# Optimization experiments

Hardware: AMD Instinct MI355X
Metric: run time of the kernel (lower is better)

Reference implementation:

```python
import jax, jax.numpy as jnp
import numpy as np

B, N, DIM = 2, 2048, 1024
HEADS, DIM_HEAD = 16, 64
ALIBI_HEADS = 8
NUM_MEM_KV = 4
SCALE = DIM_HEAD ** -0.5


def alibi_slopes(n):
    # standard ALiBi geometric slopes for power-of-2 head counts
    start = 2.0 ** (-8.0 / n)
    return jnp.array([start ** (k + 1) for k in range(n)], dtype=jnp.float32)


def alibi_bias(i, j, heads, total_heads):
    # symmetric ALiBi: bias = -|k_pos - q_pos| * slope; unbiased heads padded with zeros at front
    range_q = jnp.arange(j - i, j)          # query absolute positions (offset by mem kv)
    range_k = jnp.arange(j)
    rel = -jnp.abs(range_k[None, :] - range_q[:, None]).astype(jnp.float32)  # [i, j]
    slopes = alibi_slopes(heads)
    bias = slopes[:, None, None] * rel[None]                                  # [heads, i, j]
    pad = jnp.zeros((total_heads - heads, i, j), dtype=bias.dtype)
    return jnp.concatenate([pad, bias], axis=0)                               # [total_heads, i, j]


def setup_inputs() -> dict:
    key = jax.random.key(0)
    ks = jax.random.split(key, 7)
    w = lambda k, s: jax.random.normal(k, s, jnp.float32) * 0.02
    return {
        "x": jax.random.normal(ks[0], (B, N, DIM), jnp.float32),
        "mask": jnp.ones((B, N), dtype=bool),
        "Wq": w(ks[1], (DIM, HEADS * DIM_HEAD)),
        "Wk": w(ks[2], (DIM, HEADS * DIM_HEAD)),
        "Wv": w(ks[3], (DIM, HEADS * DIM_HEAD)),
        "Wo": w(ks[4], (HEADS * DIM_HEAD, DIM)),
        "mem_k": jax.random.normal(ks[5], (HEADS, NUM_MEM_KV, DIM_HEAD), jnp.float32),
        "mem_v": jax.random.normal(ks[6], (HEADS, NUM_MEM_KV, DIM_HEAD), jnp.float32),
    }


def reference(x, mask, Wq, Wk, Wv, Wo, mem_k, mem_v):
    b, n, _ = x.shape
    h, d, m = HEADS, DIM_HEAD, NUM_MEM_KV
    # QKV projections (Linear, no bias)
    q = (x @ Wq).reshape(b, n, h, d).transpose(0, 2, 1, 3)  # [b,h,n,d]
    k = (x @ Wk).reshape(b, n, h, d).transpose(0, 2, 1, 3)
    v = (x @ Wv).reshape(b, n, h, d).transpose(0, 2, 1, 3)
    # prepend learned memory key/values
    k = jnp.concatenate([jnp.broadcast_to(mem_k[None], (b, h, m, d)), k], axis=2)
    v = jnp.concatenate([jnp.broadcast_to(mem_v[None], (b, h, m, d)), v], axis=2)
    i, j = n, n + m
    # input mask padded with True over memory positions
    input_mask = jnp.concatenate([jnp.ones((b, m), dtype=bool), mask], axis=1)  # [b,j]
    # causal mask: key kj attendable by query qi iff kj - (j - i) <= qi (mem keys always visible)
    qpos = jnp.arange(i)[:, None]
    kpos = jnp.arange(j)[None, :]
    causal_allow = (kpos - (j - i)) <= qpos                                      # [i,j]
    allow = input_mask[:, None, None, :] & causal_allow[None, None]              # [b,1,i,j]
    bias = alibi_bias(i, j, ALIBI_HEADS, h)                                      # [h,i,j]
    scores = jnp.einsum('bhid,bhjd->bhij', q, k) * SCALE + bias[None]
    scores = jnp.where(allow, scores, jnp.finfo(scores.dtype).min)
    attn = jax.nn.softmax(scores, axis=-1)
    out = jnp.einsum('bhij,bhjd->bhid', attn, v)
    out = out.transpose(0, 2, 1, 3).reshape(b, n, h * d) @ Wo
    return out * mask[..., None].astype(out.dtype)
```

## Files before the change

### kernel.cpp

```cpp
#include <hip/hip_runtime.h>

typedef __bf16 bf16x8 __attribute__((ext_vector_type(8)));
typedef float f32x4 __attribute__((ext_vector_type(4)));
typedef unsigned short us8 __attribute__((ext_vector_type(8)));
typedef unsigned short ushort_t;
typedef unsigned int uint_t;

constexpr int BATCH = 2;
constexpr int SEQ   = 2048;
constexpr int DIM   = 1024;
constexpr int HEADS = 16;
constexpr int DH    = 64;
constexpr int NKV   = 4;
constexpr int KROWS = 2080;
constexpr int KVSTR = 133120;
constexpr float QSCALE = 0.18033688011112042f;

__device__ inline ushort_t f2bf(float f) {
  uint_t u = __builtin_bit_cast(uint_t, f);
  u += 0x7FFFu + ((u >> 16) & 1u);
  return (ushort_t)(u >> 16);
}

__device__ inline uint_t pk2bf(float a, float b) {
  return (uint_t)f2bf(a) | ((uint_t)f2bf(b) << 16);
}

__device__ inline size_t swz(int row, int k) {
  return ((size_t)(row >> 7) << 17) +
         (size_t)(((k >> 3) << 7) + (row & 127)) * 8 + (k & 7);
}

__device__ inline int koff(int j, int d) {
  return ((j >> 4) << 10) + ((d >> 3) << 7) + ((j & 15) << 3) + (d & 7);
}
__device__ inline int voff(int j, int d) {
  int w = j & 31;
  int kap = ((w & 15) << 1) | (w >> 4);
  return ((j >> 5) << 11) + ((kap >> 3) << 9) + (d << 3) + (kap & 7);
}

__device__ inline void g2l16(const ushort_t* g, ushort_t* l) {
  __builtin_amdgcn_global_load_lds(
      (const __attribute__((address_space(1))) void*)g,
      (__attribute__((address_space(3))) void*)l, 16, 0, 0);
}

__global__ __launch_bounds__(256) void prep_kernel(
    const float* __restrict__ x,
    const float* __restrict__ W0, const float* __restrict__ W1,
    const float* __restrict__ W2, const float* __restrict__ W3,
    const float* __restrict__ memk, const float* __restrict__ memv,
    ushort_t* __restrict__ xb,
    ushort_t* __restrict__ T0, ushort_t* __restrict__ T1,
    ushort_t* __restrict__ T2, ushort_t* __restrict__ T3,
    ushort_t* __restrict__ Vt, ushort_t* __restrict__ Ka)
{
  __shared__ float tile[32][33];
  int bid = blockIdx.x, t = threadIdx.x;
  if (bid < 2048) {
    int idx = bid * 256 + t;
    const float4* s = (const float4*)x;
    float4 a = s[idx * 2], bq = s[idx * 2 + 1];
    us8 o;
    o[0] = f2bf(a.x);  o[1] = f2bf(a.y);  o[2] = f2bf(a.z);  o[3] = f2bf(a.w);
    o[4] = f2bf(bq.x); o[5] = f2bf(bq.y); o[6] = f2bf(bq.z); o[7] = f2bf(bq.w);
    int e = idx * 8, row = e >> 10, k = e & 1023;
    *(us8*)&xb[swz(row, k)] = o;
  } else if (bid < 6144) {
    int tb = bid - 2048, z = tb >> 10, r2 = tb & 1023;
    int bx = r2 & 31, by = r2 >> 5;
    const float* W = (z == 0) ? W0 : (z == 1) ? W1 : (z == 2) ? W2 : W3;
    ushort_t* T = (z == 0) ? T0 : (z == 1) ? T1 : (z == 2) ? T2 : T3;
    float sc = (z == 0) ? QSCALE : 1.0f;
    int tx = t & 31, ty = t >> 5;
    int kb = bx * 32, nb = by * 32;
    for (int y = ty; y < 32; y += 8)
      tile[y][tx] = W[(size_t)(kb + y) * 1024 + nb + tx];
    __syncthreads();
    for (int y = ty; y < 32; y += 8)
      T[swz(nb + y, kb + tx)] = f2bf(tile[tx][y] * sc);
  } else {
    int idx = (bid - 6144) * 256 + t;
    if (idx < 8192) {
      int j = idx & 3, d = (idx >> 2) & 63, h = (idx >> 8) & 15, b = idx >> 12;
      Vt[(size_t)(b * 16 + h) * KVSTR + voff(j, d)] =
          f2bf(memv[((size_t)h * NKV + j) * DH + d]);
    } else if (idx < 16384) {
      int k2 = idx - 8192;
      int d = k2 & 63, j = (k2 >> 6) & 3, h = (k2 >> 8) & 15, b = k2 >> 12;
      Ka[(size_t)(b * 16 + h) * KVSTR + koff(j, d)] =
          f2bf(memk[((size_t)h * NKV + j) * DH + d]);
    }
  }
}

__global__ __launch_bounds__(256) void gemm_bt(
    const ushort_t* __restrict__ A,
    const ushort_t* __restrict__ Wt0, const ushort_t* __restrict__ Wt1,
    const ushort_t* __restrict__ Wt2,
    ushort_t* __restrict__ C0, ushort_t* __restrict__ Ka,
    ushort_t* __restrict__ Vt, float* __restrict__ Cf, int zbase)
{
  __shared__ ushort_t As[8192];
  __shared__ ushort_t Bs[8192];
  int z = blockIdx.z + zbase;
  const ushort_t* Wt = (z == 1) ? Wt1 : (z == 2) ? Wt2 : Wt0;
  int t = threadIdx.x;
  int lane = t & 63, wave = t >> 6;
  int col = lane & 15, quad = lane >> 4;
  int m0 = blockIdx.y * 128, n0 = blockIdx.x * 128;
  int moff = (wave >> 1) * 64, noff = (wave & 1) * 64;

  const ushort_t* Abase = A  + ((size_t)(m0 >> 7) << 17);
  const ushort_t* Bbase = Wt + ((size_t)(n0 >> 7) << 17);
  int so = wave * 2048 + lane * 8;

  f32x4 acc[4][4] = {};

  for (int k0 = 0; k0 < DIM; k0 += 64) {
    __syncthreads();
    const ushort_t* Ak = Abase + ((size_t)k0 << 7);
    const ushort_t* Bk = Bbase + ((size_t)k0 << 7);
#pragma unroll
    for (int c2 = 0; c2 < 4; c2++) {
      g2l16(Ak + so + c2 * 512, &As[so + c2 * 512]);
      g2l16(Bk + so + c2 * 512, &Bs[so + c2 * 512]);
    }
    __syncthreads();
#pragma unroll
    for (int kc = 0; kc < 2; kc++) {
      bf16x8 af[4], bfr[4];
#pragma unroll
      for (int mi = 0; mi < 4; mi++)
        af[mi] = *(const bf16x8*)&As[(kc * 4 + quad) * 1024 + (moff + mi * 16 + col) * 8];
#pragma unroll
      for (int ni = 0; ni < 4; ni++)
        bfr[ni] = *(const bf16x8*)&Bs[(kc * 4 + quad) * 1024 + (noff + ni * 16 + col) * 8];
#pragma unroll
      for (int mi = 0; mi < 4; mi++)
#pragma unroll
        for (int ni = 0; ni < 4; ni++)
          acc[mi][ni] = __builtin_amdgcn_mfma_f32_16x16x32_bf16(
              af[mi], bfr[ni], acc[mi][ni], 0, 0, 0);
    }
  }

  if (z == 0) {
#pragma unroll
    for (int mi = 0; mi < 4; mi++) {
      int row0 = m0 + moff + mi * 16 + quad * 4;
#pragma unroll
      for (int ni = 0; ni < 4; ni++) {
        int cn = n0 + noff + ni * 16 + col;
#pragma unroll
        for (int r = 0; r < 4; r++)
          C0[swz(row0 + r, cn)] = f2bf(acc[mi][ni][r]);
      }
    }
  } else if (z == 1) {
#pragma unroll
    for (int mi = 0; mi < 4; mi++) {
      int gi = m0 + moff + mi * 16 + quad * 4;
      int bq = gi >> 11, i = gi & 2047;
#pragma unroll
      for (int ni = 0; ni < 4; ni++) {
        int feat = n0 + noff + ni * 16 + col;
        int hh = feat >> 6, dd = feat & 63;
        size_t base = (size_t)(bq * 16 + hh) * KVSTR;
#pragma unroll
        for (int r = 0; r < 4; r++)
          Ka[base + koff(i + r + NKV, dd)] = f2bf(acc[mi][ni][r]);
      }
    }
  } else if (z == 2) {
#pragma unroll
    for (int mi = 0; mi < 4; mi++) {
      int gi = m0 + moff + mi * 16 + quad * 4;
      int bq = gi >> 11, i = gi & 2047;
#pragma unroll
      for (int ni = 0; ni < 4; ni++) {
        int feat = n0 + noff + ni * 16 + col;
        int hh = feat >> 6, dd = feat & 63;
        size_t vb = (size_t)(bq * 16 + hh) * KVSTR;
#pragma unroll
        for (int r = 0; r < 4; r++)
          Vt[vb + voff(i + r + NKV, dd)] = f2bf(acc[mi][ni][r]);
      }
    }
  } else {
#pragma unroll
    for (int mi = 0; mi < 4; mi++) {
      int row0 = m0 + moff + mi * 16 + quad * 4;
#pragma unroll
      for (int ni = 0; ni < 4; ni++) {
        int cn = n0 + noff + ni * 16 + col;
#pragma unroll
        for (int r = 0; r < 4; r++)
          Cf[(size_t)(row0 + r) * DIM + cn] = acc[mi][ni][r];
      }
    }
  }
}

__global__ __launch_bounds__(256) void attn_kernel(
    const ushort_t* __restrict__ Q, const ushort_t* __restrict__ Ka,
    const ushort_t* __restrict__ Vt, ushort_t* __restrict__ AO)
{
  __shared__ __align__(16) uint_t Plds[4][16][20];
  __shared__ __align__(16) float Cmb[2][64][20];
  int t = threadIdx.x, lane = t & 63, wave = t >> 6;
  int col = lane & 15, quad = lane >> 4;
  int bid = blockIdx.x;
  int xcd = bid & 7, slot = bid >> 3;
  int bh = xcd + 8 * (slot >> 5);
  int b = bh >> 4, h = bh & 15;
  int u = slot & 31;
  int pi = u * 2 + (wave >> 1);
  int h2 = wave & 1;
  int p2 = wave >> 1;
  float slope2 = (h < 8) ? 0.0f : exp2f(-(float)(h - 7)) * 1.4426950408889634f;

  const ushort_t* Kbh = Ka + (size_t)bh * KVSTR;
  const ushort_t* Vbh = Vt + (size_t)bh * KVSTR;

  us8 ones_u = {0x3F80, 0x3F80, 0x3F80, 0x3F80, 0x3F80, 0x3F80, 0x3F80, 0x3F80};
  bf16x8 ones = __builtin_bit_cast(bf16x8, ones_u);

  int kOff = quad * 128 + col * 8;
  int vOff = quad * 512 + col * 8;

  for (int hv = 0; hv < 2; hv++) {
    int s = hv ? 127 - pi : pi;
    int i0 = s * 16;
    int jend = ((16 * s + 51) >> 5) << 5;

    bf16x8 qa0 = *(const bf16x8*)&Q[swz(b * SEQ + i0 + col, h * DH + quad * 8)];
    bf16x8 qa1 = *(const bf16x8*)&Q[swz(b * SEQ + i0 + col, h * DH + 32 + quad * 8)];

    f32x4 o0 = {}, o1 = {}, o2 = {}, o3 = {}, ol = {};

    int vK = h2 * 2048 + kOff;
    int vV = h2 * 2048 + vOff;
    bf16x8 k00 = *(const bf16x8*)&Kbh[vK];
    bf16x8 k01 = *(const bf16x8*)&Kbh[vK + 512];
    bf16x8 k10 = *(const bf16x8*)&Kbh[vK + 1024];
    bf16x8 k11 = *(const bf16x8*)&Kbh[vK + 1536];
    bf16x8 v0 = *(const bf16x8*)&Vbh[vV];
    bf16x8 v1 = *(const bf16x8*)&Vbh[vV + 128];
    bf16x8 v2 = *(const bf16x8*)&Vbh[vV + 256];
    bf16x8 v3 = *(const bf16x8*)&Vbh[vV + 384];

    for (int jb = h2 * 32; jb < jend; jb += 64) {
      f32x4 s0 = {}, s1 = {};
      s0 = __builtin_amdgcn_mfma_f32_16x16x32_bf16(qa0, k00, s0, 0, 0, 0);
      s0 = __builtin_amdgcn_mfma_f32_16x16x32_bf16(qa1, k01, s0, 0, 0, 0);
      s1 = __builtin_amdgcn_mfma_f32_16x16x32_bf16(qa0, k10, s1, 0, 0, 0);
      s1 = __builtin_amdgcn_mfma_f32_16x16x32_bf16(qa1, k11, s1, 0, 0, 0);

      int step = (jb + 64 < jend) ? 4096 : 0;
      vK += step;
      k00 = *(const bf16x8*)&Kbh[vK];
      k01 = *(const bf16x8*)&Kbh[vK + 512];
      k10 = *(const bf16x8*)&Kbh[vK + 1024];
      k11 = *(const bf16x8*)&Kbh[vK + 1536];

      float fDb = (float)(jb + col - i0 - quad * 4 - NKV);
      if (jb <= i0 - 27) {
#pragma unroll
        for (int r = 0; r < 4; r++) {
          float fr = fDb - (float)r;
          float p0 = exp2f(fmaf(slope2, fr, s0[r]));
          float p1 = exp2f(fmaf(slope2, fr + 16.0f, s1[r]));
          Plds[wave][quad * 4 + r][col] = pk2bf(p0, p1);
        }
      } else {
#pragma unroll
        for (int r = 0; r < 4; r++) {
          float fr = fDb - (float)r, fr1 = fr + 16.0f;
          float vv0 = fmaf(slope2, fr, s0[r]);
          float vv1 = fmaf(slope2, fr1, s1[r]);
          vv0 = (fr  <= 0.0f) ? vv0 : -1e30f;
          vv1 = (fr1 <= 0.0f) ? vv1 : -1e30f;
          float p0 = exp2f(vv0), p1 = exp2f(vv1);
          Plds[wave][quad * 4 + r][col] = pk2bf(p0, p1);
        }
      }

      bf16x8 pf = *(const bf16x8*)&Plds[wave][col][quad * 4];
      o0 = __builtin_amdgcn_mfma_f32_16x16x32_bf16(pf, v0, o0, 0, 0, 0);
      o1 = __builtin_amdgcn_mfma_f32_16x16x32_bf16(pf, v1, o1, 0, 0, 0);
      o2 = __builtin_amdgcn_mfma_f32_16x16x32_bf16(pf, v2, o2, 0, 0, 0);
      o3 = __builtin_amdgcn_mfma_f32_16x16x32_bf16(pf, v3, o3, 0, 0, 0);
      ol = __builtin_amdgcn_mfma_f32_16x16x32_bf16(pf, ones, ol, 0, 0, 0);

      vV += step;
      v0 = *(const bf16x8*)&Vbh[vV];
      v1 = *(const bf16x8*)&Vbh[vV + 128];
      v2 = *(const bf16x8*)&Vbh[vV + 256];
      v3 = *(const bf16x8*)&Vbh[vV + 384];
    }

    if (h2 == 1) {
      *(f32x4*)&Cmb[p2][lane][0]  = o0;
      *(f32x4*)&Cmb[p2][lane][4]  = o1;
      *(f32x4*)&Cmb[p2][lane][8]  = o2;
      *(f32x4*)&Cmb[p2][lane][12] = o3;
      *(f32x4*)&Cmb[p2][lane][16] = ol;
    }
    __syncthreads();
    if (h2 == 0) {
      o0 += *(const f32x4*)&Cmb[p2][lane][0];
      o1 += *(const f32x4*)&Cmb[p2][lane][4];
      o2 += *(const f32x4*)&Cmb[p2][lane][8];
      o3 += *(const f32x4*)&Cmb[p2][lane][12];
      ol += *(const f32x4*)&Cmb[p2][lane][16];
#pragma unroll
      for (int r = 0; r < 4; r++) {
        float linv = __builtin_amdgcn_rcpf(ol[r]);
        int row = b * SEQ + i0 + quad * 4 + r;
        AO[swz(row, h * DH + col)]      = f2bf(o0[r] * linv);
        AO[swz(row, h * DH + 16 + col)] = f2bf(o1[r] * linv);
        AO[swz(row, h * DH + 32 + col)] = f2bf(o2[r] * linv);
        AO[swz(row, h * DH + 48 + col)] = f2bf(o3[r] * linv);
      }
    }
    __syncthreads();
  }
}

extern "C" void kernel_launch(void* const* d_in, const int* in_sizes, int n_in,
                              void* d_out, int out_size, void* d_ws, size_t ws_size,
                              hipStream_t stream)
{
  const float* x    = (const float*)d_in[0];
  const float* Wq   = (const float*)d_in[2];
  const float* Wk   = (const float*)d_in[3];
  const float* Wv   = (const float*)d_in[4];
  const float* Wo   = (const float*)d_in[5];
  const float* memk = (const float*)d_in[6];
  const float* memv = (const float*)d_in[7];
  float* out = (float*)d_out;

  char* ws = (char*)d_ws;
  size_t off = 0;
  auto alloc = [&](size_t bytes) {
    char* p = ws + off;
    off += (bytes + 255) & ~(size_t)255;
    return p;
  };
  ushort_t* WqT = (ushort_t*)alloc((size_t)1024 * 1024 * 2);
  ushort_t* WkT = (ushort_t*)alloc((size_t)1024 * 1024 * 2);
  ushort_t* WvT = (ushort_t*)alloc((size_t)1024 * 1024 * 2);
  ushort_t* WoT = (ushort_t*)alloc((size_t)1024 * 1024 * 2);
  ushort_t* xb  = (ushort_t*)alloc((size_t)4096 * 1024 * 2);
  ushort_t* Qb  = (ushort_t*)alloc((size_t)4096 * 1024 * 2);
  ushort_t* Ka  = (ushort_t*)alloc((size_t)32 * KVSTR * 2);
  ushort_t* Vt  = (ushort_t*)alloc((size_t)32 * KVSTR * 2);
  ushort_t* AO  = xb;

  prep_kernel<<<dim3(6208), dim3(256), 0, stream>>>(
      x, Wq, Wk, Wv, Wo, memk, memv, xb, WqT, WkT, WvT, WoT, Vt, Ka);
  gemm_bt<<<dim3(8, 32, 3), dim3(256), 0, stream>>>(xb, WqT, WkT, WvT, Qb, Ka, Vt, nullptr, 0);
  attn_kernel<<<dim3(1024), dim3(256), 0, stream>>>(Qb, Ka, Vt, AO);
  gemm_bt<<<dim3(8, 32, 1), dim3(256), 0, stream>>>(AO, WoT, nullptr, nullptr,
                                                    nullptr, nullptr, nullptr, out, 3);
}
```

Measured before the change: 200.1 us.

## Remap GEMM blocks per XCD and use 64-row tiles for output projection

The QKV GEMM moves to a 1D grid whose block index is decoded so that each XCD gets a contiguous region of M and N tiles, aiming to improve L2 reuse of A and W tiles within each chiplet. The output projection gets a dedicated kernel with 64x128 tiles, which doubles the block count to 512 so the CUs are better filled, plus the same XCD-aware mapping. The cost is smaller tiles with less reuse per block in the output GEMM, and A loads that read half of each 128-row packed tile.

```diff
diff --git a/kernel.cpp b/kernel.cpp
--- a/kernel.cpp
+++ b/kernel.cpp
@@ -100,16 +100,20 @@
     const ushort_t* __restrict__ Wt0, const ushort_t* __restrict__ Wt1,
     const ushort_t* __restrict__ Wt2,
     ushort_t* __restrict__ C0, ushort_t* __restrict__ Ka,
-    ushort_t* __restrict__ Vt, float* __restrict__ Cf, int zbase)
+    ushort_t* __restrict__ Vt)
 {
   __shared__ ushort_t As[8192];
   __shared__ ushort_t Bs[8192];
-  int z = blockIdx.z + zbase;
+  int bid = blockIdx.x;
+  int xcd = bid & 7, g = bid >> 3;
+  int z = g >> 5, rem = g & 31;
+  int my = (xcd >> 1) * 8 + (rem >> 2);
+  int nx = (xcd & 1) * 4 + (rem & 3);
   const ushort_t* Wt = (z == 1) ? Wt1 : (z == 2) ? Wt2 : Wt0;
   int t = threadIdx.x;
   int lane = t & 63, wave = t >> 6;
   int col = lane & 15, quad = lane >> 4;
-  int m0 = blockIdx.y * 128, n0 = blockIdx.x * 128;
+  int m0 = my * 128, n0 = nx * 128;
   int moff = (wave >> 1) * 64, noff = (wave & 1) * 64;
 
   const ushort_t* Abase = A  + ((size_t)(m0 >> 7) << 17);
@@ -173,7 +177,7 @@
           Ka[base + koff(i + r + NKV, dd)] = f2bf(acc[mi][ni][r]);
       }
     }
-  } else if (z == 2) {
+  } else {
 #pragma unroll
     for (int mi = 0; mi < 4; mi++) {
       int gi = m0 + moff + mi * 16 + quad * 4;
@@ -188,17 +192,72 @@
           Vt[vb + voff(i + r + NKV, dd)] = f2bf(acc[mi][ni][r]);
       }
     }
-  } else {
-#pragma unroll
-    for (int mi = 0; mi < 4; mi++) {
-      int row0 = m0 + moff + mi * 16 + quad * 4;
-#pragma unroll
-      for (int ni = 0; ni < 4; ni++) {
-        int cn = n0 + noff + ni * 16 + col;
-#pragma unroll
-        for (int r = 0; r < 4; r++)
-          Cf[(size_t)(row0 + r) * DIM + cn] = acc[mi][ni][r];
-      }
+  }
+}
+
+__global__ __launch_bounds__(256) void gemm_out64(
+    const ushort_t* __restrict__ A, const ushort_t* __restrict__ Wt,
+    float* __restrict__ Cf)
+{
+  __shared__ ushort_t As[4096];
+  __shared__ ushort_t Bs[8192];
+  int bid = blockIdx.x;
+  int xcd = bid & 7, g = bid >> 3;
+  int my = xcd * 8 + (g >> 3);
+  int nx = g & 7;
+  int t = threadIdx.x;
+  int lane = t & 63, wave = t >> 6;
+  int col = lane & 15, quad = lane >> 4;
+  int m0 = my * 64, n0 = nx * 128;
+  int moff = (wave >> 1) * 32, noff = (wave & 1) * 64;
+  int mhalf = my & 1;
+
+  const ushort_t* Abase = A  + ((size_t)(my >> 1) << 17);
+  const ushort_t* Bbase = Wt + ((size_t)(n0 >> 7) << 17);
+  int so = wave * 2048 + lane * 8;
+
+  f32x4 acc[2][4] = {};
+
+  for (int k0 = 0; k0 < DIM; k0 += 64) {
+    __syncthreads();
+    const ushort_t* Ak = Abase + ((size_t)k0 << 7);
+    const ushort_t* Bk = Bbase + ((size_t)k0 << 7);
+#pragma unroll
+    for (int c2 = 0; c2 < 2; c2++) {
+      int ko = wave * 2 + c2;
+      g2l16(Ak + ko * 1024 + mhalf * 512 + lane * 8, &As[ko * 512 + lane * 8]);
+    }
+#pragma unroll
+    for (int c2 = 0; c2 < 4; c2++)
+      g2l16(Bk + so + c2 * 512, &Bs[so + c2 * 512]);
+    __syncthreads();
+#pragma unroll
+    for (int kc = 0; kc < 2; kc++) {
+      bf16x8 af[2], bfr[4];
+#pragma unroll
+      for (int mi = 0; mi < 2; mi++)
+        af[mi] = *(const bf16x8*)&As[(kc * 4 + quad) * 512 + (moff + mi * 16 + col) * 8];
+#pragma unroll
+      for (int ni = 0; ni < 4; ni++)
+        bfr[ni] = *(const bf16x8*)&Bs[(kc * 4 + quad) * 1024 + (noff + ni * 16 + col) * 8];
+#pragma unroll
+      for (int mi = 0; mi < 2; mi++)
+#pragma unroll
+        for (int ni = 0; ni < 4; ni++)
+          acc[mi][ni] = __builtin_amdgcn_mfma_f32_16x16x32_bf16(
+              af[mi], bfr[ni], acc[mi][ni], 0, 0, 0);
+    }
+  }
+
+#pragma unroll
+  for (int mi = 0; mi < 2; mi++) {
+    int row0 = m0 + moff + mi * 16 + quad * 4;
+#pragma unroll
+    for (int ni = 0; ni < 4; ni++) {
+      int cn = n0 + noff + ni * 16 + col;
+#pragma unroll
+      for (int r = 0; r < 4; r++)
+        Cf[(size_t)(row0 + r) * DIM + cn] = acc[mi][ni][r];
     }
   }
 }
@@ -361,8 +420,7 @@
 
   prep_kernel<<<dim3(6208), dim3(256), 0, stream>>>(
       x, Wq, Wk, Wv, Wo, memk, memv, xb, WqT, WkT, WvT, WoT, Vt, Ka);
-  gemm_bt<<<dim3(8, 32, 3), dim3(256), 0, stream>>>(xb, WqT, WkT, WvT, Qb, Ka, Vt, nullptr, 0);
+  gemm_bt<<<dim3(768), dim3(256), 0, stream>>>(xb, WqT, WkT, WvT, Qb, Ka, Vt);
   attn_kernel<<<dim3(1024), dim3(256), 0, stream>>>(Qb, Ka, Vt, AO);
-  gemm_bt<<<dim3(8, 32, 1), dim3(256), 0, stream>>>(AO, WoT, nullptr, nullptr,
-                                                    nullptr, nullptr, nullptr, out, 3);
-}
+  gemm_out64<<<dim3(512), dim3(256), 0, stream>>>(AO, WoT, out);
+}
```

Measured after the change: 191.5 us. -4.3%, faster.
